# Performance work log

Measured on AMD Instinct MI355X. Metric: run time of the kernel, lower is better.

## Reference

```python
import math
import jax, jax.numpy as jnp
import numpy as np

NUM_PRE_NMS = 2000
NMS_THR = 0.7
MIN_SIZE = 16.0
LOG_MAX = math.log(1000.0 / 16)  # clamp on dh, dw as in the torch module

B, A, H, W = 8, 3, 200, 304
STRIDE = 4


def _make_anchors():
    # grid anchors, channel-last anchor ordering to match permute(0,2,3,1)
    sizes = np.array([32.0, 64.0, 128.0], dtype=np.float32)  # A sizes
    ys = (np.arange(H, dtype=np.float32) + 0.5) * STRIDE
    xs = (np.arange(W, dtype=np.float32) + 0.5) * STRIDE
    cy, cx = np.meshgrid(ys, xs, indexing="ij")  # [H,W]
    cx = cx[:, :, None]
    cy = cy[:, :, None]
    half = (sizes / 2.0)[None, None, :]  # [1,1,A]
    anc = np.stack([cx - half, cy - half, cx + half, cy + half], axis=-1)  # [H,W,A,4]
    anc = anc.reshape(-1, 4)  # [H*W*A, 4]
    anc = np.broadcast_to(anc[None], (B, anc.shape[0], 4)).copy()
    return jnp.asarray(anc)


def setup_inputs() -> dict:
    key = jax.random.key(0)
    k1, k2 = jax.random.split(key)
    cls_logits = jax.random.normal(k1, (B, A, H, W), dtype=jnp.float32)
    regs = jax.random.normal(k2, (B, 4 * A, H, W), dtype=jnp.float32) * 0.1
    anchors = _make_anchors()
    return {"cls_logits": cls_logits, "regs": regs, "anchors": anchors,
            "image_h": 800, "image_w": 1216}


def _box_iou(boxes):
    # boxes: [K,4] -> iou [K,K]
    x1, y1, x2, y2 = boxes[:, 0], boxes[:, 1], boxes[:, 2], boxes[:, 3]
    area = (x2 - x1) * (y2 - y1)
    ix1 = jnp.maximum(x1[:, None], x1[None, :])
    iy1 = jnp.maximum(y1[:, None], y1[None, :])
    ix2 = jnp.minimum(x2[:, None], x2[None, :])
    iy2 = jnp.minimum(y2[:, None], y2[None, :])
    iw = jnp.clip(ix2 - ix1, 0.0)
    ih = jnp.clip(iy2 - iy1, 0.0)
    inter = iw * ih
    union = area[:, None] + area[None, :] - inter
    return inter / jnp.maximum(union, 1e-6)


def _nms_one(boxes, valid):
    # boxes sorted by descending score; greedy suppression, fixed-size keep mask
    k = boxes.shape[0]
    iou = _box_iou(boxes)
    later = jnp.arange(k)

    def body(i, keep):
        sup = (iou[i] > NMS_THR) & keep[i] & (later > i)
        return keep & ~sup

    return jax.lax.fori_loop(0, k, body, valid)


def reference(cls_logits, regs, anchors, image_h, image_w):
    b = cls_logits.shape[0]
    # scores/regs in channel-last anchor order (matches permute(0,2,3,1))
    scores = jnp.transpose(cls_logits, (0, 2, 3, 1)).reshape(b, -1)       # [B,N]
    deltas = jnp.transpose(regs, (0, 2, 3, 1)).reshape(b, -1, 4)          # [B,N,4]
    n = scores.shape[1]
    k = min(NUM_PRE_NMS, n)

    top_scores, idx = jax.lax.top_k(scores, k)                            # [B,K]
    top_deltas = jnp.take_along_axis(deltas, idx[:, :, None], axis=1)     # [B,K,4]
    top_anchors = jnp.take_along_axis(anchors, idx[:, :, None], axis=1)   # [B,K,4]

    dx, dy = top_deltas[..., 0], top_deltas[..., 1]
    dh = jnp.minimum(top_deltas[..., 2], LOG_MAX)
    dw = jnp.minimum(top_deltas[..., 3], LOG_MAX)
    ah = top_anchors[..., 3] - top_anchors[..., 1]
    aw = top_anchors[..., 2] - top_anchors[..., 0]
    cx = aw / 2
    cy = ah / 2
    px = cx + dx * aw
    py = cy + dy * ah
    ph = jnp.exp(dh) * ah
    pw = jnp.exp(dw) * aw
    boxes = jnp.stack([px - pw / 2, py - ph / 2, px + pw / 2, py + ph / 2], axis=-1)  # [B,K,4]

    # size filter on clamped coords (as in _nms)
    w_img = jnp.float32(image_w)
    h_img = jnp.float32(image_h)
    bw = jnp.clip(boxes[..., 2], 0.0, w_img) - jnp.clip(boxes[..., 0], 0.0, w_img)
    bh = jnp.clip(boxes[..., 3], 0.0, h_img) - jnp.clip(boxes[..., 1], 0.0, h_img)
    valid = (bw >= MIN_SIZE) & (bh >= MIN_SIZE)

    keep = jax.vmap(_nms_one)(boxes, valid)                               # [B,K]
    out_boxes = boxes * keep[..., None].astype(boxes.dtype)
    return out_boxes, top_scores, keep
```

## Files before the change

### kernel.cpp

```cpp
#include <hip/hip_runtime.h>

#define HWSZ 60800
#define NA 3
#define NTOT 182400
#define KSEL 2000
#define CANDCAP 8192
#define SELCAP 4096
#define NBATCH 8
#define GSPLIT 128
#define LOG_MAX_F 4.135166556742356f

#define OFF_H1    0
#define OFF_CCNT  65536
#define OFF_SCNT  65568
#define ZR_BYTES  65600
#define OFF_SEL   65600
#define OFF_BOX   65728
#define OFF_VALID 321728
#define OFF_SUP   385728
#define OFF_CAND  385728
#define OFF_SELK  910016

__device__ __forceinline__ unsigned int xform(float f) {
    unsigned int b = __float_as_uint(f);
    return b ^ ((unsigned int)((int)b >> 31) | 0x80000000u);
}

__global__ __launch_bounds__(256) void k_hist1(const float* __restrict__ cls,
                                               unsigned int* __restrict__ hist1) {
    int b = blockIdx.y, part = blockIdx.x, tid = threadIdx.x;
    __shared__ unsigned int h[2048];
    for (int i = tid; i < 2048; i += 256) h[i] = 0u;
    __syncthreads();
    const float4* base4 = (const float4*)(cls + (size_t)b * NTOT);
    const int n4 = NTOT / 4;
    int per = (n4 + GSPLIT - 1) / GSPLIT;
    int lo = part * per, hi = lo + per;
    if (hi > n4) hi = n4;
    for (int i = lo + tid; i < hi; i += 256) {
        float4 v = base4[i];
        atomicAdd(&h[xform(v.x) >> 21], 1u);
        atomicAdd(&h[xform(v.y) >> 21], 1u);
        atomicAdd(&h[xform(v.z) >> 21], 1u);
        atomicAdd(&h[xform(v.w) >> 21], 1u);
    }
    __syncthreads();
    unsigned int* gh = hist1 + b * 2048;
    for (int i = tid; i < 2048; i += 256)
        if (h[i]) atomicAdd(&gh[i], h[i]);
}

__global__ __launch_bounds__(1024) void k_scan1(const unsigned int* __restrict__ hist1,
                                                uint4* __restrict__ selinfo) {
    int b = blockIdx.x, tid = threadIdx.x;
    __shared__ unsigned int sa[2048], sb[2048];
    const unsigned int* h = hist1 + b * 2048;
    sa[tid] = h[tid];
    sa[tid + 1024] = h[tid + 1024];
    unsigned int* src = sa; unsigned int* dst = sb;
    for (int d = 1; d < 2048; d <<= 1) {
        __syncthreads();
        dst[tid] = src[tid] + ((tid + d < 2048) ? src[tid + d] : 0u);
        int i2 = tid + 1024;
        dst[i2] = src[i2] + ((i2 + d < 2048) ? src[i2 + d] : 0u);
        unsigned int* t = src; src = dst; dst = t;
    }
    __syncthreads();
    #pragma unroll
    for (int k = 0; k < 2; ++k) {
        int i = tid + k * 1024;
        unsigned int c = src[i];
        unsigned int cn = (i < 2047) ? src[i + 1] : 0u;
        if (c >= KSEL && cn < KSEL)
            selinfo[b] = make_uint4((unsigned int)i, cn, KSEL - cn, 0u);
    }
}

__global__ __launch_bounds__(256) void k_gather(const float* __restrict__ cls,
                                                const uint4* __restrict__ selinfo,
                                                unsigned long long* __restrict__ cand,
                                                unsigned int* __restrict__ ccnt) {
    int b = blockIdx.y, part = blockIdx.x, tid = threadIdx.x;
    unsigned int bin = selinfo[b].x;
    __shared__ unsigned long long lbuf[1024];
    __shared__ unsigned int lcnt, gbase;
    if (tid == 0) lcnt = 0u;
    __syncthreads();
    const float4* base4 = (const float4*)(cls + (size_t)b * NTOT);
    const int n4 = NTOT / 4;
    int per = (n4 + GSPLIT - 1) / GSPLIT;
    int lo = part * per, hi = lo + per;
    if (hi > n4) hi = n4;
    for (int i = lo + tid; i < hi; i += 256) {
        float4 v = base4[i];
        float vals[4] = {v.x, v.y, v.z, v.w};
        int idx0 = i * 4;
        #pragma unroll
        for (int q = 0; q < 4; ++q) {
            unsigned int u = xform(vals[q]);
            if ((u >> 21) >= bin) {
                int idx = idx0 + q;
                int a = idx / HWSZ;
                int hw = idx - a * HWSZ;
                unsigned int n = (unsigned int)(hw * NA + a);
                unsigned int pos = atomicAdd(&lcnt, 1u);
                if (pos < 1024u)
                    lbuf[pos] = ((unsigned long long)u << 32) | (unsigned long long)(~n);
            }
        }
    }
    __syncthreads();
    if (tid == 0) {
        unsigned int c = lcnt < 1024u ? lcnt : 1024u;
        gbase = atomicAdd(&ccnt[b], c);
    }
    __syncthreads();
    unsigned int c = lcnt < 1024u ? lcnt : 1024u;
    unsigned int gb = gbase;
    for (unsigned int i = tid; i < c; i += 256) {
        unsigned int p = gb + i;
        if (p < CANDCAP) cand[(size_t)b * CANDCAP + p] = lbuf[i];
    }
}

__global__ __launch_bounds__(1024) void k_refine(const unsigned long long* __restrict__ cand,
                                                 const unsigned int* __restrict__ ccnt,
                                                 const uint4* __restrict__ selinfo,
                                                 unsigned long long* __restrict__ selk,
                                                 unsigned int* __restrict__ scnt) {
    int b = blockIdx.x;
    int tid = threadIdx.x;
    __shared__ unsigned int sa[2048], sb[2048];
    __shared__ unsigned int acnt, shT;
    uint4 si = selinfo[b];
    unsigned int bin = si.x, krem = si.z;
    unsigned int m = ccnt[b];
    if (m > CANDCAP) m = CANDCAP;
    const unsigned long long* cb = cand + (size_t)b * CANDCAP;

    sa[tid] = 0u; sa[tid + 1024] = 0u;
    if (tid == 0) acnt = 0u;
    __syncthreads();
    for (unsigned int i = tid; i < m; i += 1024) {
        unsigned int u = (unsigned int)(cb[i] >> 32);
        if ((u >> 21) == bin) atomicAdd(&sa[(u >> 10) & 2047u], 1u);
    }
    unsigned int* src = sa; unsigned int* dst = sb;
    for (int d = 1; d < 2048; d <<= 1) {
        __syncthreads();
        dst[tid] = src[tid] + ((tid + d < 2048) ? src[tid + d] : 0u);
        int i2 = tid + 1024;
        dst[i2] = src[i2] + ((i2 + d < 2048) ? src[i2 + d] : 0u);
        unsigned int* t = src; src = dst; dst = t;
    }
    __syncthreads();
    #pragma unroll
    for (int k = 0; k < 2; ++k) {
        int i = tid + k * 1024;
        unsigned int c = src[i];
        unsigned int cn = (i < 2047) ? src[i + 1] : 0u;
        if (c >= krem && cn < krem)
            shT = (bin << 21) | ((unsigned int)i << 10);
    }
    __syncthreads();
    unsigned int T = shT;

    int lane = tid & 63;
    unsigned long long lmask = (1ULL << lane) - 1ULL;
    unsigned int mr = (m + 1023u) & ~1023u;
    unsigned long long* sout = selk + (size_t)b * SELCAP;
    for (unsigned int i = tid; i < mr; i += 1024) {
        bool pred = false;
        unsigned long long key = 0ULL;
        if (i < m) {
            key = cb[i];
            pred = ((unsigned int)(key >> 32)) >= T;
        }
        unsigned long long mask = __ballot(pred);
        unsigned int cw = (unsigned int)__popcll(mask);
        unsigned int base = 0u;
        if (lane == 0 && cw) base = atomicAdd(&acnt, cw);
        base = __shfl(base, 0, 64);
        if (pred) {
            unsigned int pos = base + (unsigned int)__popcll(mask & lmask);
            if (pos < SELCAP) sout[pos] = key;
        }
    }
    __syncthreads();
    if (tid == 0) scnt[b] = (acnt < SELCAP) ? acnt : SELCAP;
}

__global__ __launch_bounds__(256) void k_rank_decode(
        const unsigned long long* __restrict__ selk,
        const unsigned int* __restrict__ scnt,
        const float* __restrict__ regs,
        const float* __restrict__ anchors,
        const int* __restrict__ img_h,
        const int* __restrict__ img_w,
        float* __restrict__ out_scores,
        float4* __restrict__ boxes_ws,
        unsigned int* __restrict__ valid_ws) {
    int b = blockIdx.y;
    int tid = threadIdx.x;
    int lane = tid & 63;
    unsigned int sc = scnt[b];
    if (sc > SELCAP) sc = SELCAP;
    unsigned int r = blockIdx.x * 256 + tid;
    if (blockIdx.x * 256 >= sc) return;
    const unsigned long long* sb_ = selk + (size_t)b * SELCAP;
    unsigned long long mykey = (r < sc) ? sb_[r] : 0ULL;

    unsigned int cnt = 0u;
    for (unsigned int base = 0; base < sc; base += 64) {
        unsigned long long kj = 0ULL;
        if (base + (unsigned int)lane < sc) kj = sb_[base + lane];
        unsigned int klo = (unsigned int)kj;
        unsigned int khi = (unsigned int)(kj >> 32);
        #pragma unroll
        for (int t = 0; t < 64; ++t) {
            unsigned int lo = (unsigned int)__builtin_amdgcn_readlane((int)klo, t);
            unsigned int hi = (unsigned int)__builtin_amdgcn_readlane((int)khi, t);
            unsigned long long kt = ((unsigned long long)hi << 32) | (unsigned long long)lo;
            cnt += (kt > mykey) ? 1u : 0u;
        }
    }
    if (r >= sc || cnt >= KSEL) return;

    int hv = img_h[0];
    int wv = img_w[0];
    float himg = (hv > 0 && hv < 100000) ? (float)hv : __int_as_float(hv);
    float wimg = (wv > 0 && wv < 100000) ? (float)wv : __int_as_float(wv);

    unsigned int u = (unsigned int)(mykey >> 32);
    unsigned int n = ~((unsigned int)mykey);
    unsigned int bits = (u & 0x80000000u) ? (u & 0x7FFFFFFFu) : ~u;
    float score = __uint_as_float(bits);
    int a = (int)(n % NA);
    int hw = (int)(n / NA);
    const float* rp = regs + ((size_t)b * (4 * NA) + 4 * a) * HWSZ + hw;
    float dx = rp[0 * HWSZ];
    float dy = rp[1 * HWSZ];
    float dh = rp[2 * HWSZ];
    float dw = rp[3 * HWSZ];
    const float* ap = anchors + ((size_t)b * NTOT + n) * 4;
    float ax1 = ap[0], ay1 = ap[1], ax2 = ap[2], ay2 = ap[3];
    float ahh = ay2 - ay1;
    float aww = ax2 - ax1;
    float cx = aww * 0.5f;
    float cy = ahh * 0.5f;
    float px = cx + dx * aww;
    float py = cy + dy * ahh;
    dh = fminf(dh, LOG_MAX_F);
    dw = fminf(dw, LOG_MAX_F);
    float ph = expf(dh) * ahh;
    float pw = expf(dw) * aww;
    float x1 = px - pw * 0.5f;
    float y1 = py - ph * 0.5f;
    float x2 = px + pw * 0.5f;
    float y2 = py + ph * 0.5f;
    float bwv = fminf(fmaxf(x2, 0.f), wimg) - fminf(fmaxf(x1, 0.f), wimg);
    float bhv = fminf(fmaxf(y2, 0.f), himg) - fminf(fmaxf(y1, 0.f), himg);
    unsigned int valid = (bwv >= 16.f && bhv >= 16.f) ? 1u : 0u;
    size_t o = (size_t)b * KSEL + cnt;
    out_scores[o] = score;
    boxes_ws[o] = make_float4(x1, y1, x2, y2);
    valid_ws[o] = valid;
}

__global__ __launch_bounds__(256) void k_supmat(const float4* __restrict__ boxes_ws,
                                                unsigned long long* __restrict__ sup) {
    int ct = blockIdx.x;
    int rt = blockIdx.y;
    int b  = blockIdx.z;
    int tid = threadIdx.x;
    __shared__ float4 colbox[64];
    int j0 = ct * 64;
    if (tid < 64) {
        int jl = j0 + tid;
        colbox[tid] = (jl < KSEL) ? boxes_ws[(size_t)b * KSEL + jl]
                                  : make_float4(0.f, 0.f, 0.f, 0.f);
    }
    __syncthreads();
    int i = rt * 256 + tid;
    if (i >= KSEL) return;
    float4 bi = boxes_ws[(size_t)b * KSEL + i];
    float area_i = (bi.z - bi.x) * (bi.w - bi.y);
    unsigned long long word = 0ULL;
    #pragma unroll 8
    for (int jj = 0; jj < 64; ++jj) {
        int j = j0 + jj;
        float4 bj = colbox[jj];
        float area_j = (bj.z - bj.x) * (bj.w - bj.y);
        float ix1 = fmaxf(bi.x, bj.x);
        float iy1 = fmaxf(bi.y, bj.y);
        float ix2 = fminf(bi.z, bj.z);
        float iy2 = fminf(bi.w, bj.w);
        float iw = fmaxf(ix2 - ix1, 0.f);
        float ih = fmaxf(iy2 - iy1, 0.f);
        float inter = iw * ih;
        float uni = area_i + area_j - inter;
        float iou = inter / fmaxf(uni, 1e-6f);
        bool s = (j > i) && (j < KSEL) && (iou > 0.7f);
        if (s) word |= (1ULL << jj);
    }
    sup[((size_t)b * KSEL + i) * 32 + ct] = word;
}

#define LOAD_TILE(wnext, buf)                                                \
    {                                                                        \
        int gbase_ = (wnext) * 2048;                                         \
        _Pragma("unroll")                                                    \
        for (int k = 0; k < 8; ++k) {                                        \
            int e_ = tid + k * 256;                                          \
            int row_ = (wnext) * 64 + (e_ >> 5);                             \
            buf[k] = (row_ < KSEL) ? srow[gbase_ + e_] : 0ULL;               \
        }                                                                    \
    }

#define PROCESS_TILE(w, buf)                                                 \
    {                                                                        \
        if (myword == (w)) {                                                 \
            _Pragma("unroll")                                                \
            for (int k = 0; k < 8; ++k)                                      \
                diag[(tid >> 5) + k * 8] = buf[k];                           \
        }                                                                    \
        __syncthreads();      \
        unsigned long long dval_ = diag[lane];                               \
        unsigned int dlo_ = (unsigned int)dval_;                             \
        unsigned int dhi_ = (unsigned int)(dval_ >> 32);                     \
        unsigned long long pend_ =                                           \
            ((unsigned long long)accw[(w) * 2 + 1] << 32)                    \
            | (unsigned long long)accw[(w) * 2];                             \
        unsigned long long c64_ = kws[w] & ~pend_;                           \
        unsigned int clo_ = __builtin_amdgcn_readfirstlane((unsigned int)c64_);        \
        unsigned int chi_ = __builtin_amdgcn_readfirstlane((unsigned int)(c64_ >> 32));\
        unsigned long long cur_ = ((unsigned long long)chi_ << 32)           \
                                  | (unsigned long long)clo_;                \
        if (cur_) {                                                          \
            unsigned long long rem_ = cur_;                                  \
            while (rem_) {      \
                int bit_ = __builtin_ctzll(rem_);                            \
                unsigned int lo_ = (unsigned int)__builtin_amdgcn_readlane((int)dlo_, bit_); \
                unsigned int hi_ = (unsigned int)__builtin_amdgcn_readlane((int)dhi_, bit_); \
                unsigned long long d_ = ((unsigned long long)hi_ << 32)      \
                                        | (unsigned long long)lo_;           \
                cur_ &= ~d_;                                                 \
                rem_ = cur_ & ~((2ULL << bit_) - 1ULL);                      \
            }                                                                \
            if (tid == 0) fin[w] = cur_;                                     \
            unsigned long long v_ = 0ULL;                                    \
            _Pragma("unroll")                                                \
            for (int k = 0; k < 8; ++k) {                                    \
                int row_ = (tid >> 5) + k * 8;                               \
                if ((cur_ >> row_) & 1ULL) v_ |= buf[k];                     \
            }                                                                \
            v_ |= __shfl_xor(v_, 32, 64);                                    \
            if (lane < 32 && v_) {                                           \
                atomicOr(&accw[myword * 2], (unsigned int)v_);               \
                atomicOr(&accw[myword * 2 + 1], (unsigned int)(v_ >> 32));   \
            }                                                                \
        } else if (tid == 0) {                                               \
            fin[w] = 0ULL;                                                   \
        }                                                                    \
    }

__global__ __launch_bounds__(256) void k_nms_scan(const unsigned long long* __restrict__ sup,
                                                  const unsigned int* __restrict__ valid_ws,
                                                  const float4* __restrict__ boxes_ws,
                                                  float* __restrict__ out_boxes,
                                                  float* __restrict__ out_keep) {
    int b = blockIdx.x;
    int tid = threadIdx.x;
    int lane = tid & 63;
    int myword = tid & 31;
    __shared__ unsigned long long kws[32];
    __shared__ unsigned long long fin[32];
    __shared__ unsigned long long diag[64];
    __shared__ unsigned int accw[64];
    const unsigned long long* srow = sup + (size_t)b * KSEL * 32;

    if (tid < 32) {
        unsigned long long kw = 0ULL;
        const uint4* vv = (const uint4*)(valid_ws + (size_t)b * KSEL);
        #pragma unroll 4
        for (int q = 0; q < 16; ++q) {
            uint4 x = vv[tid * 16 + q];
            int base = q * 4;
            if (x.x) kw |= 1ULL << (base + 0);
            if (x.y) kw |= 1ULL << (base + 1);
            if (x.z) kw |= 1ULL << (base + 2);
            if (x.w) kw |= 1ULL << (base + 3);
        }
        if (tid == 31) kw &= 0xFFFFULL;
        kws[tid] = kw;
    }
    if (tid < 64) accw[tid] = 0u;

    unsigned long long A[8], B[8];
    LOAD_TILE(0, A);
    LOAD_TILE(1, B);

    for (int t = 0; t < 16; ++t) {
        int w = 2 * t;
        PROCESS_TILE(w, A);
        if (w + 2 < 32) LOAD_TILE(w + 2, A);
        PROCESS_TILE(w + 1, B);
        if (w + 3 < 32) LOAD_TILE(w + 3, B);
    }
    __syncthreads();

    for (int r = tid; r < KSEL; r += 256) {
        float kf = (float)((fin[r >> 6] >> (r & 63)) & 1ULL);
        size_t o = (size_t)b * KSEL + r;
        out_keep[o] = kf;
        float4 bx = boxes_ws[o];
        float* ob = out_boxes + o * 4;
        ob[0] = bx.x * kf;
        ob[1] = bx.y * kf;
        ob[2] = bx.z * kf;
        ob[3] = bx.w * kf;
    }
}

extern "C" void kernel_launch(void* const* d_in, const int* in_sizes, int n_in,
                              void* d_out, int out_size, void* d_ws, size_t ws_size,
                              hipStream_t stream) {
    const float* cls     = (const float*)d_in[0];
    const float* regs    = (const float*)d_in[1];
    const float* anchors = (const float*)d_in[2];
    const int*   img_h   = (const int*)d_in[3];
    const int*   img_w   = (const int*)d_in[4];

    float* out = (float*)d_out;
    float* out_boxes  = out;
    float* out_scores = out + 64000;
    float* out_keep   = out + 80000;

    char* ws = (char*)d_ws;
    unsigned int* hist1      = (unsigned int*)(ws + OFF_H1);
    unsigned int* ccnt       = (unsigned int*)(ws + OFF_CCNT);
    unsigned int* scnt       = (unsigned int*)(ws + OFF_SCNT);
    uint4* selinfo           = (uint4*)(ws + OFF_SEL);
    float4* boxes_ws         = (float4*)(ws + OFF_BOX);
    unsigned int* valid_ws   = (unsigned int*)(ws + OFF_VALID);
    unsigned long long* sup  = (unsigned long long*)(ws + OFF_SUP);
    unsigned long long* cand = (unsigned long long*)(ws + OFF_CAND);
    unsigned long long* selk = (unsigned long long*)(ws + OFF_SELK);

    hipMemsetAsync(ws, 0, ZR_BYTES, stream);
    k_hist1<<<dim3(GSPLIT, NBATCH), 256, 0, stream>>>(cls, hist1);
    k_scan1<<<NBATCH, 1024, 0, stream>>>(hist1, selinfo);
    k_gather<<<dim3(GSPLIT, NBATCH), 256, 0, stream>>>(cls, selinfo, cand, ccnt);
    k_refine<<<NBATCH, 1024, 0, stream>>>(cand, ccnt, selinfo, selk, scnt);
    k_rank_decode<<<dim3(10, NBATCH), 256, 0, stream>>>(selk, scnt, regs, anchors,
                                                        img_h, img_w, out_scores,
                                                        boxes_ws, valid_ws);
    k_supmat<<<dim3(32, 8, NBATCH), 256, 0, stream>>>(boxes_ws, sup);
    k_nms_scan<<<NBATCH, 256, 0, stream>>>(sup, valid_ws, boxes_ws, out_boxes, out_keep);
}
```

Before: 220.3 us.

## Split rank counting across four waves per key block; skip empty diagonal rows in NMS

```diff
diff --git a/kernel.cpp b/kernel.cpp
--- a/kernel.cpp
+++ b/kernel.cpp
@@ -202,29 +202,42 @@
         unsigned int* __restrict__ valid_ws) {
     int b = blockIdx.y;
     int tid = threadIdx.x;
-    int lane = tid & 63;
     unsigned int sc = scnt[b];
     if (sc > SELCAP) sc = SELCAP;
-    unsigned int r = blockIdx.x * 256 + tid;
-    if (blockIdx.x * 256 >= sc) return;
+    unsigned int kbase = blockIdx.x * 64;
+    if (kbase >= sc) return;
+    int ki = tid & 63;
+    int q = tid >> 6;
+    int lane = tid & 63;
     const unsigned long long* sb_ = selk + (size_t)b * SELCAP;
+    unsigned int r = kbase + (unsigned int)ki;
     unsigned long long mykey = (r < sc) ? sb_[r] : 0ULL;
 
+    unsigned int qs = ((sc + 255u) >> 8) << 6;
+    unsigned int lo = (unsigned int)q * qs;
+    unsigned int hi = lo + qs;
+    if (hi > sc) hi = sc;
+
     unsigned int cnt = 0u;
-    for (unsigned int base = 0; base < sc; base += 64) {
+    for (unsigned int base = lo; base < hi; base += 64) {
         unsigned long long kj = 0ULL;
-        if (base + (unsigned int)lane < sc) kj = sb_[base + lane];
+        if (base + (unsigned int)lane < hi) kj = sb_[base + lane];
         unsigned int klo = (unsigned int)kj;
         unsigned int khi = (unsigned int)(kj >> 32);
         #pragma unroll
         for (int t = 0; t < 64; ++t) {
-            unsigned int lo = (unsigned int)__builtin_amdgcn_readlane((int)klo, t);
-            unsigned int hi = (unsigned int)__builtin_amdgcn_readlane((int)khi, t);
-            unsigned long long kt = ((unsigned long long)hi << 32) | (unsigned long long)lo;
+            unsigned int lo_ = (unsigned int)__builtin_amdgcn_readlane((int)klo, t);
+            unsigned int hi_ = (unsigned int)__builtin_amdgcn_readlane((int)khi, t);
+            unsigned long long kt = ((unsigned long long)hi_ << 32) | (unsigned long long)lo_;
             cnt += (kt > mykey) ? 1u : 0u;
         }
     }
-    if (r >= sc || cnt >= KSEL) return;
+    __shared__ unsigned int cntsh[4][64];
+    cntsh[q][ki] = cnt;
+    __syncthreads();
+    if (tid >= 64) return;
+    unsigned int rank = cntsh[0][ki] + cntsh[1][ki] + cntsh[2][ki] + cntsh[3][ki];
+    if (r >= sc || rank >= KSEL) return;
 
     int hv = img_h[0];
     int wv = img_w[0];
@@ -261,7 +274,7 @@
     float bwv = fminf(fmaxf(x2, 0.f), wimg) - fminf(fmaxf(x1, 0.f), wimg);
     float bhv = fminf(fmaxf(y2, 0.f), himg) - fminf(fmaxf(y1, 0.f), himg);
     unsigned int valid = (bwv >= 16.f && bhv >= 16.f) ? 1u : 0u;
-    size_t o = (size_t)b * KSEL + cnt;
+    size_t o = (size_t)b * KSEL + rank;
     out_scores[o] = score;
     boxes_ws[o] = make_float4(x1, y1, x2, y2);
     valid_ws[o] = valid;
@@ -326,6 +339,7 @@
         }                                                                    \
         __syncthreads();      \
         unsigned long long dval_ = diag[lane];                               \
+        unsigned long long nz_ = __ballot(dval_ != 0ULL);                    \
         unsigned int dlo_ = (unsigned int)dval_;                             \
         unsigned int dhi_ = (unsigned int)(dval_ >> 32);                     \
         unsigned long long pend_ =                                           \
@@ -337,15 +351,16 @@
         unsigned long long cur_ = ((unsigned long long)chi_ << 32)           \
                                   | (unsigned long long)clo_;                \
         if (cur_) {                                                          \
-            unsigned long long rem_ = cur_;                                  \
-            while (rem_) {      \
+             \
+            unsigned long long rem_ = cur_ & nz_;                            \
+            while (rem_) {                                                   \
                 int bit_ = __builtin_ctzll(rem_);                            \
                 unsigned int lo_ = (unsigned int)__builtin_amdgcn_readlane((int)dlo_, bit_); \
                 unsigned int hi_ = (unsigned int)__builtin_amdgcn_readlane((int)dhi_, bit_); \
                 unsigned long long d_ = ((unsigned long long)hi_ << 32)      \
                                         | (unsigned long long)lo_;           \
                 cur_ &= ~d_;                                                 \
-                rem_ = cur_ & ~((2ULL << bit_) - 1ULL);                      \
+                rem_ = cur_ & nz_ & ~((2ULL << bit_) - 1ULL);                \
             }                                                                \
             if (tid == 0) fin[w] = cur_;                                     \
             unsigned long long v_ = 0ULL;                                    \
@@ -452,9 +467,9 @@
     k_scan1<<<NBATCH, 1024, 0, stream>>>(hist1, selinfo);
     k_gather<<<dim3(GSPLIT, NBATCH), 256, 0, stream>>>(cls, selinfo, cand, ccnt);
     k_refine<<<NBATCH, 1024, 0, stream>>>(cand, ccnt, selinfo, selk, scnt);
-    k_rank_decode<<<dim3(10, NBATCH), 256, 0, stream>>>(selk, scnt, regs, anchors,
-                                                        img_h, img_w, out_scores,
-                                                        boxes_ws, valid_ws);
+    k_rank_decode<<<dim3(SELCAP / 64, NBATCH), 256, 0, stream>>>(selk, scnt, regs, anchors,
+                                                                 img_h, img_w, out_scores,
+                                                                 boxes_ws, valid_ws);
     k_supmat<<<dim3(32, 8, NBATCH), 256, 0, stream>>>(boxes_ws, sup);
     k_nms_scan<<<NBATCH, 256, 0, stream>>>(sup, valid_ws, boxes_ws, out_boxes, out_keep);
 }
```

New measurement: 199.6 us, median of 2. 9.4% less time.
